# Performance work log

Hardware: AMD Instinct MI355X
Metric: run time of the kernel (lower is better)

The kernel has to match this reference:

```python
import jax, jax.numpy as jnp
import numpy as np

TAU = 0.02  # softmax temperature (logits are divided by tau)


def setup_inputs() -> dict:
    key = jax.random.key(0)
    k1, k2 = jax.random.split(key)
    B, N, H, W = 4, 256, 256, 256
    H_img, W_img = 512, 512
    logits = jax.random.normal(k1, (B, N, H, W), dtype=jnp.float32)
    # ground-truth match coordinates (x, y) in image-pixel space
    gt_xy = jax.random.uniform(k2, (B, N, 2), dtype=jnp.float32) * jnp.array(
        [W_img - 1, H_img - 1], dtype=jnp.float32
    )
    # grid buffer: (H*W, 2) rows of (x, y), x fastest (meshgrid ij, stacked [xs, ys])
    ys, xs = jnp.meshgrid(jnp.arange(H), jnp.arange(W), indexing="ij")
    grid = jnp.stack([xs, ys], axis=-1).reshape(-1, 2).astype(jnp.float32)
    return {"logits": logits, "gt_xy": gt_xy, "grid": grid, "H_img": H_img, "W_img": W_img}


def reference(logits, gt_xy, grid, H_img, W_img):
    B, N, H, W = logits.shape
    # scale gt coords from image pixels to feature-map pixels (per-axis (new-1)/(old-1))
    scale_in = jnp.array([(W - 1) / (W_img - 1), (H - 1) / (H_img - 1)], dtype=logits.dtype)
    gt_fm = gt_xy * scale_in  # (B, N, 2)
    # temperature softmax over flattened spatial dim
    prob = jax.nn.softmax(logits.reshape(B, N, H * W) / TAU, axis=-1)  # (B, N, HW)
    # soft-argmax: expected (x, y) coordinate
    pred = jnp.einsum("bnl,lc->bnc", prob, grid)  # (B, N, 2)
    norm_scale = jnp.array([W - 1, H - 1], dtype=pred.dtype)
    pred_norm = 2.0 * pred / norm_scale - 1.0
    gt_norm = 2.0 * gt_fm / norm_scale - 1.0
    err = jnp.linalg.norm(pred_norm - gt_norm, axis=-1)  # (B, N)
    return err.sum()
```

## Files before the change

kernel.cpp:

```cpp
#include <hip/hip_runtime.h>
#include <math.h>

#define TAU_INV 50.0f

__device__ __forceinline__ void osm_merge(float& m, float& s, float& sx, float& sy,
                                          float m2, float s2, float sx2, float sy2) {
    float nm = fmaxf(m, m2);
    float c1 = __expf(m - nm);
    float c2 = __expf(m2 - nm);
    s  = s  * c1 + s2  * c2;
    sx = sx * c1 + sx2 * c2;
    sy = sy * c1 + sy2 * c2;
    m = nm;
}

__global__ __launch_bounds__(256) void soft_argmax_rows(
        const float* __restrict__ logits,
        const float* __restrict__ gt_xy,
        const int* __restrict__ HimgP,
        const int* __restrict__ WimgP,
        float* __restrict__ row_err,
        int W, int H) {
    const int row = blockIdx.x;
    const int HW  = W * H;
    const int tid = threadIdx.x;
    const float4* b4 = (const float4*)(logits + (size_t)row * (size_t)HW);
    const int nvec = HW >> 2;

    float m = -INFINITY, s = 0.f, sx = 0.f, sy = 0.f;

    for (int i = tid; i < nvec; i += 256) {
        float4 v = b4[i];
        int l0 = i << 2;
        int y  = l0 / W;
        int x0 = l0 - y * W;
        float fy = (float)y;
        float vv[4] = {v.x, v.y, v.z, v.w};
        #pragma unroll
        for (int j = 0; j < 4; ++j) {
            float a  = vv[j] * TAU_INV;
            float fx = (float)(x0 + j);
            if (a <= m) {
                float w = __expf(a - m);
                s  += w;
                sx += w * fx;
                sy += w * fy;
            } else {
                float c = __expf(m - a);
                s  = s  * c + 1.f;
                sx = sx * c + fx;
                sy = sy * c + fy;
                m = a;
            }
        }
    }

    #pragma unroll
    for (int off = 32; off >= 1; off >>= 1) {
        float m2  = __shfl_xor(m,  off);
        float s2  = __shfl_xor(s,  off);
        float sx2 = __shfl_xor(sx, off);
        float sy2 = __shfl_xor(sy, off);
        osm_merge(m, s, sx, sy, m2, s2, sx2, sy2);
    }

    __shared__ float sm[4], ss[4], ssx[4], ssy[4];
    const int wave = tid >> 6, lane = tid & 63;
    if (lane == 0) { sm[wave] = m; ss[wave] = s; ssx[wave] = sx; ssy[wave] = sy; }
    __syncthreads();

    if (tid == 0) {
        #pragma unroll
        for (int wv = 1; wv < 4; ++wv)
            osm_merge(m, s, sx, sy, sm[wv], ss[wv], ssx[wv], ssy[wv]);
        float px = sx / s;
        float py = sy / s;
        float Wimg = (float)WimgP[0];
        float Himg = (float)HimgP[0];
        float gxf = gt_xy[2 * row + 0] * ((float)(W - 1) / (Wimg - 1.f));
        float gyf = gt_xy[2 * row + 1] * ((float)(H - 1) / (Himg - 1.f));
        float dx = 2.f * (px - gxf) / (float)(W - 1);
        float dy = 2.f * (py - gyf) / (float)(H - 1);
        row_err[row] = sqrtf(dx * dx + dy * dy);
    }
}

__global__ __launch_bounds__(256) void sum_rows(const float* __restrict__ row_err,
                                                float* __restrict__ out, int n) {
    const int tid = threadIdx.x;
    float acc = 0.f;
    for (int i = tid; i < n; i += 256) acc += row_err[i];
    #pragma unroll
    for (int off = 32; off >= 1; off >>= 1) acc += __shfl_xor(acc, off);
    __shared__ float sw[4];
    const int wave = tid >> 6, lane = tid & 63;
    if (lane == 0) sw[wave] = acc;
    __syncthreads();
    if (tid == 0) out[0] = sw[0] + sw[1] + sw[2] + sw[3];
}

extern "C" void kernel_launch(void* const* d_in, const int* in_sizes, int n_in,
                              void* d_out, int out_size, void* d_ws, size_t ws_size,
                              hipStream_t stream) {
    const float* logits = (const float*)d_in[0];
    const float* gt_xy  = (const float*)d_in[1];
    const int*   HimgP  = (const int*)d_in[3];
    const int*   WimgP  = (const int*)d_in[4];

    const int HW = in_sizes[2] / 2;
    const int BN = in_sizes[1] / 2;
    int W = 1;
    while (W * W < HW) W <<= 1;
    if (W * W != HW) W = (int)(sqrtf((float)HW) + 0.5f);
    const int H = HW / W;

    float* row_err = (float*)d_ws;
    float* out     = (float*)d_out;

    soft_argmax_rows<<<BN, 256, 0, stream>>>(logits, gt_xy, HimgP, WimgP, row_err, W, H);
    sum_rows<<<1, 256, 0, stream>>>(row_err, out, BN);
}
```

Before: 54.72 us.

## Split each softmax row across two blocks and merge partials in finish kernel

Each row is now processed by two blocks that each cover half of the spatial elements and write (max, sum, sx, sy) partials. The single finish kernel merges the two partials per row and computes the error and sum. The inner loop also changes: two float4 loads are issued per iteration, the branchy online-softmax update becomes a branchless form with two exps per element, and the per-vector integer division is replaced by a float reciprocal with a correction step. This doubles block count to improve occupancy and latency hiding on a memory-bound pass, but the extra exp per element adds ALU work.

```diff
diff --git a/kernel.cpp b/kernel.cpp
--- a/kernel.cpp
+++ b/kernel.cpp
@@ -11,47 +11,62 @@
     s  = s  * c1 + s2  * c2;
     sx = sx * c1 + sx2 * c2;
     sy = sy * c1 + sy2 * c2;
-    m = nm;
+    m  = nm;
 }
 
-__global__ __launch_bounds__(256) void soft_argmax_rows(
+__device__ __forceinline__ void osm_elem(float& m, float& s, float& sx, float& sy,
+                                         float a, float fx, float fy) {
+    float nm = fmaxf(m, a);
+    float c  = __expf(m - nm);
+    float w  = __expf(a - nm);
+    s  = fmaf(s,  c, w);
+    sx = fmaf(sx, c, w * fx);
+    sy = fmaf(sy, c, w * fy);
+    m  = nm;
+}
+
+__global__ __launch_bounds__(256) void soft_argmax_part(
         const float* __restrict__ logits,
-        const float* __restrict__ gt_xy,
-        const int* __restrict__ HimgP,
-        const int* __restrict__ WimgP,
-        float* __restrict__ row_err,
-        int W, int H) {
-    const int row = blockIdx.x;
-    const int HW  = W * H;
+        float4* __restrict__ part,
+        int W, int elems_per_blk, float invW) {
+    const int blk = blockIdx.x;
     const int tid = threadIdx.x;
-    const float4* b4 = (const float4*)(logits + (size_t)row * (size_t)HW);
-    const int nvec = HW >> 2;
+    const int nvec = elems_per_blk >> 2;
+    const float4* b4 = (const float4*)logits + (size_t)blk * (size_t)nvec;
+    const int base_l = (blk & 1) * elems_per_blk;
 
     float m = -INFINITY, s = 0.f, sx = 0.f, sy = 0.f;
 
-    for (int i = tid; i < nvec; i += 256) {
-        float4 v = b4[i];
-        int l0 = i << 2;
-        int y  = l0 / W;
-        int x0 = l0 - y * W;
-        float fy = (float)y;
-        float vv[4] = {v.x, v.y, v.z, v.w};
-        #pragma unroll
-        for (int j = 0; j < 4; ++j) {
-            float a  = vv[j] * TAU_INV;
-            float fx = (float)(x0 + j);
-            if (a <= m) {
-                float w = __expf(a - m);
-                s  += w;
-                sx += w * fx;
-                sy += w * fy;
-            } else {
-                float c = __expf(m - a);
-                s  = s  * c + 1.f;
-                sx = sx * c + fx;
-                sy = sy * c + fy;
-                m = a;
-            }
+    for (int i = tid; i < nvec; i += 512) {
+        const int i1 = i + 256;
+        float4 v0 = b4[i];
+        float4 v1;
+        bool have1 = (i1 < nvec);
+        if (have1) v1 = b4[i1];
+
+        {
+            int l0 = base_l + (i << 2);
+            int y0 = (int)((float)l0 * invW);
+            if (y0 * W > l0) --y0;
+            else if ((y0 + 1) * W <= l0) ++y0;
+            int x0 = l0 - y0 * W;
+            float fy = (float)y0;
+            osm_elem(m, s, sx, sy, v0.x * TAU_INV, (float)(x0 + 0), fy);
+            osm_elem(m, s, sx, sy, v0.y * TAU_INV, (float)(x0 + 1), fy);
+            osm_elem(m, s, sx, sy, v0.z * TAU_INV, (float)(x0 + 2), fy);
+            osm_elem(m, s, sx, sy, v0.w * TAU_INV, (float)(x0 + 3), fy);
+        }
+        if (have1) {
+            int l0 = base_l + (i1 << 2);
+            int y0 = (int)((float)l0 * invW);
+            if (y0 * W > l0) --y0;
+            else if ((y0 + 1) * W <= l0) ++y0;
+            int x0 = l0 - y0 * W;
+            float fy = (float)y0;
+            osm_elem(m, s, sx, sy, v1.x * TAU_INV, (float)(x0 + 0), fy);
+            osm_elem(m, s, sx, sy, v1.y * TAU_INV, (float)(x0 + 1), fy);
+            osm_elem(m, s, sx, sy, v1.z * TAU_INV, (float)(x0 + 2), fy);
+            osm_elem(m, s, sx, sy, v1.w * TAU_INV, (float)(x0 + 3), fy);
         }
     }
 
@@ -73,23 +88,39 @@
         #pragma unroll
         for (int wv = 1; wv < 4; ++wv)
             osm_merge(m, s, sx, sy, sm[wv], ss[wv], ssx[wv], ssy[wv]);
-        float px = sx / s;
-        float py = sy / s;
-        float Wimg = (float)WimgP[0];
-        float Himg = (float)HimgP[0];
-        float gxf = gt_xy[2 * row + 0] * ((float)(W - 1) / (Wimg - 1.f));
-        float gyf = gt_xy[2 * row + 1] * ((float)(H - 1) / (Himg - 1.f));
-        float dx = 2.f * (px - gxf) / (float)(W - 1);
-        float dy = 2.f * (py - gyf) / (float)(H - 1);
-        row_err[row] = sqrtf(dx * dx + dy * dy);
+        part[blk] = make_float4(m, s, sx, sy);
     }
 }
 
-__global__ __launch_bounds__(256) void sum_rows(const float* __restrict__ row_err,
-                                                float* __restrict__ out, int n) {
+__global__ __launch_bounds__(256) void finish(
+        const float4* __restrict__ part,
+        const float* __restrict__ gt_xy,
+        const int* __restrict__ HimgP,
+        const int* __restrict__ WimgP,
+        float* __restrict__ out,
+        int W, int H, int BN) {
     const int tid = threadIdx.x;
+    const float Wimg = (float)WimgP[0];
+    const float Himg = (float)HimgP[0];
+    const float sxin = (float)(W - 1) / (Wimg - 1.f);
+    const float syin = (float)(H - 1) / (Himg - 1.f);
+    const float nx = 2.f / (float)(W - 1);
+    const float ny = 2.f / (float)(H - 1);
+
     float acc = 0.f;
-    for (int i = tid; i < n; i += 256) acc += row_err[i];
+    for (int r = tid; r < BN; r += 256) {
+        float4 p0 = part[2 * r + 0];
+        float4 p1 = part[2 * r + 1];
+        float m = p0.x, s = p0.y, sx = p0.z, sy = p0.w;
+        osm_merge(m, s, sx, sy, p1.x, p1.y, p1.z, p1.w);
+        float px = sx / s;
+        float py = sy / s;
+        float gx = gt_xy[2 * r + 0] * sxin;
+        float gy = gt_xy[2 * r + 1] * syin;
+        float dx = (px - gx) * nx;
+        float dy = (py - gy) * ny;
+        acc += sqrtf(dx * dx + dy * dy);
+    }
     #pragma unroll
     for (int off = 32; off >= 1; off >>= 1) acc += __shfl_xor(acc, off);
     __shared__ float sw[4];
@@ -114,9 +145,11 @@
     if (W * W != HW) W = (int)(sqrtf((float)HW) + 0.5f);
     const int H = HW / W;
 
-    float* row_err = (float*)d_ws;
-    float* out     = (float*)d_out;
+    float4* part = (float4*)d_ws;
+    float*  out  = (float*)d_out;
 
-    soft_argmax_rows<<<BN, 256, 0, stream>>>(logits, gt_xy, HimgP, WimgP, row_err, W, H);
-    sum_rows<<<1, 256, 0, stream>>>(row_err, out, BN);
+    const int elems_per_blk = HW / 2;
+    soft_argmax_part<<<2 * BN, 256, 0, stream>>>(logits, part, W, elems_per_blk,
+                                                 1.0f / (float)W);
+    finish<<<1, 256, 0, stream>>>(part, gt_xy, HimgP, WimgP, out, W, H, BN);
 }
```

Result: faster. 51.90 us (-5.2%).
